# Performance work log

Measured on AMD Instinct MI355X. Metric: run time of the kernel, lower is better.

## Reference

```python
import jax, jax.numpy as jnp
import numpy as np

H, SK, SV, PK, PV = 8, 16, 16, 4, 8
EPS = 1e-8
NUM_LOGITS = 3
SCALE_SCALAR = (NUM_LOGITS * SK) ** -0.5
SCALE_POINT = (NUM_LOGITS * PK * (9.0 / 2.0)) ** -0.5
SCALE_PAIR = NUM_LOGITS ** -0.5


def setup_inputs() -> dict:
    key = jax.random.key(0)
    ks = jax.random.split(key, 16)
    b, n, dim, pdim = 1, 512, 384, 128
    s = 0.02
    return {
        "single_repr": jax.random.normal(ks[0], (b, n, dim), jnp.float32),
        "pairwise_repr": jax.random.normal(ks[1], (b, n, n, pdim), jnp.float32),
        "rotations": jax.random.normal(ks[2], (b, n, 3, 3), jnp.float32),
        "translations": jax.random.normal(ks[3], (b, n, 3), jnp.float32),
        "Wsq": jax.random.normal(ks[4], (dim, H * SK), jnp.float32) * s,
        "Wsk": jax.random.normal(ks[5], (dim, H * SK), jnp.float32) * s,
        "Wsv": jax.random.normal(ks[6], (dim, H * SV), jnp.float32) * s,
        "Wpq": jax.random.normal(ks[7], (dim, H * PK * 3), jnp.float32) * s,
        "Wpk": jax.random.normal(ks[8], (dim, H * PK * 3), jnp.float32) * s,
        "Wpv": jax.random.normal(ks[9], (dim, H * PV * 3), jnp.float32) * s,
        "point_weights": jnp.log(jnp.exp(jnp.ones((H,), jnp.float32)) - 1.0),
        "Wpair": jax.random.normal(ks[10], (pdim, H), jnp.float32) * s,
        "bpair": jnp.zeros((H,), jnp.float32),
        "Wout": jax.random.normal(ks[11], (H * (SV + pdim + PV * 4), dim), jnp.float32) * s,
        "bout": jnp.zeros((dim,), jnp.float32),
    }


def reference(single_repr, pairwise_repr, rotations, translations,
              Wsq, Wsk, Wsv, Wpq, Wpk, Wpv, point_weights, Wpair, bpair, Wout, bout):
    x = single_repr
    b, n, _ = x.shape

    # scalar q/k/v: [b, n, h, d]
    q_s = (x @ Wsq).reshape(b, n, H, SK)
    k_s = (x @ Wsk).reshape(b, n, H, SK)
    v_s = (x @ Wsv).reshape(b, n, H, SV)

    # point q/k/v in local frame: [b, n, h, d, 3], then rotate + translate to global frame
    def to_global(t, d):
        p = t.reshape(b, n, H, d, 3)
        return jnp.einsum('bnhdc,bncr->bnhdr', p, rotations) + translations[:, :, None, None, :]

    q_p = to_global(x @ Wpq, PK)   # [b,n,h,pk,3]
    k_p = to_global(x @ Wpk, PK)
    v_p = to_global(x @ Wpv, PV)   # [b,n,h,pv,3]

    # scalar logits [b,h,i,j]
    logits_scalar = jnp.einsum('bihd,bjhd->bhij', q_s, k_s) * SCALE_SCALAR

    # point-distance logits: sum over (d,c) of (q_i - k_j)^2
    q_ph = jnp.transpose(q_p, (0, 2, 1, 3, 4))  # [b,h,i,pk,3]
    k_ph = jnp.transpose(k_p, (0, 2, 1, 3, 4))
    diff = q_ph[:, :, :, None] - k_ph[:, :, None]          # [b,h,i,j,pk,3]
    dist2 = jnp.sum(diff * diff, axis=(-2, -1))            # [b,h,i,j]
    pw = jax.nn.softplus(point_weights)[None, :, None, None]
    logits_points = -0.5 * pw * SCALE_POINT * dist2

    # pairwise bias logits
    logits_pair = jnp.transpose(pairwise_repr @ Wpair + bpair, (0, 3, 1, 2)) * SCALE_PAIR

    attn = jax.nn.softmax(logits_scalar + logits_points + logits_pair, axis=-1)  # [b,h,i,j]

    # scalar output
    res_scalar = jnp.einsum('bhij,bjhd->bihd', attn, v_s).reshape(b, n, H * SV)

    # pairwise output
    res_pair = jnp.einsum('bhij,bijd->bihd', attn, pairwise_repr).reshape(b, n, -1)

    # point output: attend, then map back to local frame with R^T
    v_ph = jnp.transpose(v_p, (0, 2, 1, 3, 4))             # [b,h,j,pv,3]
    res_p = jnp.einsum('bhij,bhjdc->bhidc', attn, v_ph)    # [b,h,i,pv,3] (global)
    res_p = res_p - translations[:, None, :, None, :]
    res_p = jnp.einsum('bhndc,bnrc->bhndr', res_p, rotations)  # R^T applied
    res_p_norm = jnp.sqrt(jnp.sum(res_p * res_p, axis=-1) + EPS)  # [b,h,n,pv]
    res_p = jnp.transpose(res_p, (0, 2, 1, 3, 4)).reshape(b, n, H * PV * 3)
    res_p_norm = jnp.transpose(res_p_norm, (0, 2, 1, 3)).reshape(b, n, H * PV)

    results = jnp.concatenate([res_scalar, res_p, res_p_norm, res_pair], axis=-1)
    return results @ Wout + bout
```

## Files before the change

### kernel.cpp

```cpp
#include <hip/hip_runtime.h>
#include <math.h>

#define NTOK 512
#define DIM 384
#define PDIM 128
#define H 8

#define QKB_STRIDE 224
#define VB_STRIDE  320
#define RES_STRIDE 1408
#define PART_STRIDE 1360

static constexpr float SCALE_SCALAR = 0.14433756729740643f;
static constexpr float SCALE_POINT  = 0.13608276348795434f;
static constexpr float SCALE_PAIR   = 0.57735026918962580f;

__device__ __forceinline__ float f4get(const float4& v, int k) {
  return (k == 0) ? v.x : (k == 1) ? v.y : (k == 2) ? v.z : v.w;
}

__global__ __launch_bounds__(192) void ipa_proj(
    const float* __restrict__ x, const float* __restrict__ rot, const float* __restrict__ trans,
    const float* __restrict__ Wsq, const float* __restrict__ Wsk, const float* __restrict__ Wsv,
    const float* __restrict__ Wpq, const float* __restrict__ Wpk, const float* __restrict__ Wpv,
    float* __restrict__ qB, float* __restrict__ kB, float* __restrict__ vB)
{
  const int tt = blockIdx.x, cg = blockIdx.y, tid = threadIdx.x;
  __shared__ float s_x[8][DIM];
  __shared__ float s_p[8][192];
  __shared__ float s_R[8][9];
  __shared__ float s_T[8][3];

#pragma unroll
  for (int tok = 0; tok < 8; ++tok)
    for (int k = tid; k < DIM; k += 192) s_x[tok][k] = x[(size_t)(tt * 8 + tok) * DIM + k];
  if (tid < 72) s_R[tid / 9][tid % 9] = rot[(size_t)(tt * 8) * 9 + tid];
  if (tid < 24) s_T[tid / 3][tid % 3] = trans[(size_t)(tt * 8) * 3 + tid];
  __syncthreads();

  const int c = cg * 192 + tid;
  const float* W; int ncols, lc;
  if      (c < 128) { W = Wsq; ncols = 128; lc = c; }
  else if (c < 256) { W = Wsk; ncols = 128; lc = c - 128; }
  else if (c < 384) { W = Wsv; ncols = 128; lc = c - 256; }
  else if (c < 480) { W = Wpq; ncols = 96;  lc = c - 384; }
  else if (c < 576) { W = Wpk; ncols = 96;  lc = c - 480; }
  else              { W = Wpv; ncols = 192; lc = c - 576; }

  float acc[8] = {};
  const float* wp = W + lc;
#pragma unroll 4
  for (int k = 0; k < DIM; ++k) {
    float w = *wp; wp += ncols;
#pragma unroll
    for (int tok = 0; tok < 8; ++tok) acc[tok] += w * s_x[tok][k];
  }

  if (cg < 2) {
#pragma unroll
    for (int tok = 0; tok < 8; ++tok) {
      const int i = tt * 8 + tok;
      if (c < 128)      qB[(size_t)i * QKB_STRIDE + c] = acc[tok];
      else if (c < 256) kB[(size_t)i * QKB_STRIDE + (c - 128)] = acc[tok];
      else              vB[(size_t)i * VB_STRIDE + (c - 256)] = acc[tok];
    }
  } else {
#pragma unroll
    for (int tok = 0; tok < 8; ++tok) s_p[tok][tid] = acc[tok];
    __syncthreads();
    for (int t = tid; t < 512; t += 192) {
      const int tok = t >> 6, tr = t & 63;
      const int i = tt * 8 + tok;
      const float* R = s_R[tok];
      const float* T = s_T[tok];
      const float* src; float* dst;
      if (cg == 2) {
        if (tr < 32) { src = &s_p[tok][tr * 3];            dst = qB + (size_t)i * QKB_STRIDE + 128 + tr * 3; }
        else         { src = &s_p[tok][96 + (tr - 32) * 3]; dst = kB + (size_t)i * QKB_STRIDE + 128 + (tr - 32) * 3; }
      } else {
        src = &s_p[tok][tr * 3]; dst = vB + (size_t)i * VB_STRIDE + 128 + tr * 3;
      }
      float px = src[0], py = src[1], pz = src[2];
#pragma unroll
      for (int r = 0; r < 3; ++r)
        dst[r] = px * R[0 * 3 + r] + py * R[1 * 3 + r] + pz * R[2 * 3 + r] + T[r];
    }
  }
}

__global__ __launch_bounds__(256, 8) void ipa_attn_part(
    const float* __restrict__ pair, const float* __restrict__ pw,
    const float* __restrict__ Wpair, const float* __restrict__ bpair,
    const float* __restrict__ qB, const float* __restrict__ kB,
    const float* __restrict__ vB, float* __restrict__ partial,
    int NC, int JR)
{
  const int i = blockIdx.x, c = blockIdx.y, tid = threadIdx.x;
  extern __shared__ float sm[];
  float* s_attn = sm;
  float* s_red  = s_attn + JR * 12;
  float* s_wp   = s_red + 2048;
  float* s_qs   = s_wp + 1024;
  float* s_qp   = s_qs + 128;
  float* s_coef = s_qp + 96;
  float* s_bp   = s_coef + 8;
  float* s_m    = s_bp + 8;
  float* s_l    = s_m + 8;

  for (int t = tid; t < 1024; t += 256) s_wp[t] = Wpair[t];
  if (tid < 224) {
    float v = qB[(size_t)i * QKB_STRIDE + tid];
    if (tid < 128) s_qs[tid] = v; else s_qp[tid - 128] = v;
  }
  if (tid < 8) {
    s_coef[tid] = -0.5f * log1pf(__expf(pw[tid])) * SCALE_POINT;
    s_bp[tid]   = bpair[tid] * SCALE_PAIR;
  }
  __syncthreads();

  {
    const int half = tid & 1;
    const int hb = half * 4;
    for (int jl = tid >> 1; jl < JR; jl += 128) {
      const int j = c * JR + jl;
      const float4* pr = reinterpret_cast<const float4*>(pair + ((size_t)i * NTOK + j) * PDIM);
      const float4* kb = reinterpret_cast<const float4*>(kB + (size_t)j * QKB_STRIDE);

      float pa[H] = {};
#pragma unroll 4
      for (int d4i = 0; d4i < 16; ++d4i) {
        const int d4 = half * 16 + d4i;
        float4 a = pr[d4];
        const float4* wp = reinterpret_cast<const float4*>(s_wp + d4 * 32);
#pragma unroll
        for (int dd = 0; dd < 4; ++dd) {
          float4 wA = wp[dd * 2], wB = wp[dd * 2 + 1];
          float xv = f4get(a, dd);
          pa[0] += xv * wA.x; pa[1] += xv * wA.y; pa[2] += xv * wA.z; pa[3] += xv * wA.w;
          pa[4] += xv * wB.x; pa[5] += xv * wB.y; pa[6] += xv * wB.z; pa[7] += xv * wB.w;
        }
      }

      float sa[4] = {};
      const float4* q4 = reinterpret_cast<const float4*>(s_qs);
#pragma unroll
      for (int t = 0; t < 16; ++t) {
        const int t4 = half * 16 + t;
        float4 q = q4[t4], k = kb[t4];
        sa[t >> 2] += q.x * k.x + q.y * k.y + q.z * k.z + q.w * k.w;
      }

      float da[4] = {};
      const float4* qp4 = reinterpret_cast<const float4*>(s_qp);
#pragma unroll
      for (int t = 0; t < 12; ++t) {
        const int t4 = half * 12 + t;
        float4 q = qp4[t4], k = kb[32 + t4];
        float d0 = q.x - k.x, d1 = q.y - k.y, d2 = q.z - k.z, d3 = q.w - k.w;
        da[t / 3] += d0 * d0 + d1 * d1 + d2 * d2 + d3 * d3;
      }

      float lg[H];
#pragma unroll
      for (int h = 0; h < H; ++h) lg[h] = pa[h] * SCALE_PAIR;
#pragma unroll
      for (int hh = 0; hh < 4; ++hh)
        lg[hb + hh] += sa[hh] * SCALE_SCALAR + s_coef[hb + hh] * da[hh];
#pragma unroll
      for (int h = 0; h < H; ++h) { float o = __shfl_xor(lg[h], 1); lg[h] += o; }
      if (half == 0) {
#pragma unroll
        for (int h = 0; h < H; ++h) s_attn[jl * 12 + h] = lg[h] + s_bp[h];
      }
    }
  }
  __syncthreads();

  {
    const int h = tid >> 5, l = tid & 31;
    float m = -1e30f;
    for (int k = l; k < JR; k += 32) m = fmaxf(m, s_attn[k * 12 + h]);
#pragma unroll
    for (int off = 16; off; off >>= 1) m = fmaxf(m, __shfl_xor(m, off, 32));
    float s = 0.f;
    for (int k = l; k < JR; k += 32) {
      float e = __expf(s_attn[k * 12 + h] - m);
      s_attn[k * 12 + h] = e;
      s += e;
    }
#pragma unroll
    for (int off = 16; off; off >>= 1) s += __shfl_xor(s, off, 32);
    if (l == 0) { s_m[h] = m; s_l[h] = s; }
  }
  __syncthreads();

  float* part = partial + ((size_t)i * NC + c) * PART_STRIDE;

  {
    const int g = tid >> 5, d4 = tid & 31;
    float4 acc[H];
#pragma unroll
    for (int h = 0; h < H; ++h) acc[h] = make_float4(0.f, 0.f, 0.f, 0.f);
    const float4* pb4 = reinterpret_cast<const float4*>(pair + (size_t)i * NTOK * PDIM);
    const int rpg = JR >> 3;
    for (int jl = g * rpg, e = g * rpg + rpg; jl < e; ++jl) {
      float4 pv = pb4[(size_t)(c * JR + jl) * 32 + d4];
      const float4* ar = reinterpret_cast<const float4*>(s_attn + jl * 12);
      float4 aA = ar[0], aB = ar[1];
#define FMA4(A, S) { (A).x += (S) * pv.x; (A).y += (S) * pv.y; (A).z += (S) * pv.z; (A).w += (S) * pv.w; }
      FMA4(acc[0], aA.x) FMA4(acc[1], aA.y) FMA4(acc[2], aA.z) FMA4(acc[3], aA.w)
      FMA4(acc[4], aB.x) FMA4(acc[5], aB.y) FMA4(acc[6], aB.z) FMA4(acc[7], aB.w)
#undef FMA4
    }
    float* buf = s_red + (g >> 2) * 1024;
    const int rnd = g & 3;
    for (int r = 0; r < 4; ++r) {
      if (rnd == r) {
        if (r == 0) {
#pragma unroll
          for (int h = 0; h < H; ++h)
            *reinterpret_cast<float4*>(buf + h * 128 + d4 * 4) = acc[h];
        } else {
#pragma unroll
          for (int h = 0; h < H; ++h) {
            float4* p = reinterpret_cast<float4*>(buf + h * 128 + d4 * 4);
            float4 v = *p;
            v.x += acc[h].x; v.y += acc[h].y; v.z += acc[h].z; v.w += acc[h].w;
            *p = v;
          }
        }
      }
      __syncthreads();
    }
    float4 v0 = *reinterpret_cast<float4*>(s_red + tid * 4);
    float4 v1 = *reinterpret_cast<float4*>(s_red + 1024 + tid * 4);
    float4 o;
    o.x = v0.x + v1.x; o.y = v0.y + v1.y; o.z = v0.z + v1.z; o.w = v0.w + v1.w;
    *reinterpret_cast<float4*>(part + 336 + tid * 4) = o;
    if (tid < 8) { part[tid] = s_m[tid]; part[8 + tid] = s_l[tid]; }
  }

  {
    const int o = tid;
    const int h0 = (o < 128) ? (o >> 4) : (o - 128) / 24;
    const int o2 = tid + 256;
    const int h1 = (tid < 64) ? (o2 - 128) / 24 : 0;
    float a0 = 0.f, a1 = 0.f;
#pragma unroll 4
    for (int jl = 0; jl < JR; ++jl) {
      const float* vr = vB + (size_t)(c * JR + jl) * VB_STRIDE;
      const float* aw = s_attn + jl * 12;
      a0 += aw[h0] * vr[o];
      if (tid < 64) a1 += aw[h1] * vr[o2];
    }
    if (o < 128) part[16 + o] = a0; else part[144 + (o - 128)] = a0;
    if (tid < 64) part[144 + (o2 - 128)] = a1;
  }
}

__global__ __launch_bounds__(256) void ipa_combine(
    const float* __restrict__ partial, const float* __restrict__ rot,
    const float* __restrict__ trans, float* __restrict__ results, int NC)
{
  const int i = blockIdx.x, tid = threadIdx.x;
  __shared__ float s_f[4][H];
  __shared__ float s_invL[H];
  __shared__ float s_res[RES_STRIDE];
  __shared__ float s_pt[192];
  __shared__ float s_R[9], s_T[3];

  const float* pb = partial + (size_t)i * NC * PART_STRIDE;
  if (tid < H) {
    float M = -1e30f;
    for (int cc = 0; cc < NC; ++cc) M = fmaxf(M, pb[cc * PART_STRIDE + tid]);
    float L = 0.f;
    for (int cc = 0; cc < NC; ++cc) {
      float f = __expf(pb[cc * PART_STRIDE + tid] - M);
      s_f[cc][tid] = f;
      L += f * pb[cc * PART_STRIDE + 8 + tid];
    }
    s_invL[tid] = 1.f / L;
  }
  if (tid >= 32 && tid < 41) s_R[tid - 32] = rot[i * 9 + (tid - 32)];
  if (tid >= 48 && tid < 51) s_T[tid - 48] = trans[i * 3 + (tid - 48)];
  __syncthreads();

  for (int idx = tid; idx < 1344; idx += 256) {
    int h, ofs;
    if (idx < 128)      { h = idx >> 4;          ofs = 16 + idx; }
    else if (idx < 320) { h = (idx - 128) / 24;  ofs = 144 + (idx - 128); }
    else                { h = (idx - 320) >> 7;  ofs = 336 + (idx - 320); }
    float v = 0.f;
    for (int cc = 0; cc < NC; ++cc) v += s_f[cc][h] * pb[cc * PART_STRIDE + ofs];
    v *= s_invL[h];
    if (idx < 128)      s_res[idx] = v;
    else if (idx < 320) s_pt[idx - 128] = v;
    else                s_res[384 + (idx - 320)] = v;
  }
  __syncthreads();

  if (tid < 64) {
    const int h = tid >> 3, p = tid & 7;
    const int base = h * 24 + p * 3;
    float gx = s_pt[base]     - s_T[0];
    float gy = s_pt[base + 1] - s_T[1];
    float gz = s_pt[base + 2] - s_T[2];
    float lx = gx * s_R[0] + gy * s_R[1] + gz * s_R[2];
    float ly = gx * s_R[3] + gy * s_R[4] + gz * s_R[5];
    float lz = gx * s_R[6] + gy * s_R[7] + gz * s_R[8];
    s_res[128 + base]     = lx;
    s_res[128 + base + 1] = ly;
    s_res[128 + base + 2] = lz;
    s_res[320 + h * 8 + p] = sqrtf(lx * lx + ly * ly + lz * lz + 1e-8f);
  }
  __syncthreads();

  float4* dst = reinterpret_cast<float4*>(results + (size_t)i * RES_STRIDE);
  const float4* src = reinterpret_cast<const float4*>(s_res);
  for (int t = tid; t < RES_STRIDE / 4; t += 256) dst[t] = src[t];
}

__global__ __launch_bounds__(256) void ipa_out(
    const float* __restrict__ results, const float* __restrict__ Wout,
    const float* __restrict__ bout, float* __restrict__ out)
{
  const int tt = blockIdx.x, ct = blockIdx.y, tid = threadIdx.x;
  __shared__ float s_a[16][128];
  __shared__ float s_w[128][32];
  const int cc = tid & 31, tr = tid >> 5;
  float acc0 = 0.f, acc1 = 0.f;
  for (int k0 = 0; k0 < RES_STRIDE; k0 += 128) {
    __syncthreads();
    for (int t = tid; t < 512; t += 256) {
      const int tok = t >> 5, k4 = t & 31;
      reinterpret_cast<float4*>(&s_a[tok][0])[k4] =
          *reinterpret_cast<const float4*>(results + (size_t)(tt * 16 + tok) * RES_STRIDE + k0 + k4 * 4);
    }
    for (int t = tid; t < 1024; t += 256) {
      const int kk = t >> 3, c4 = t & 7;
      reinterpret_cast<float4*>(&s_w[kk][0])[c4] =
          *reinterpret_cast<const float4*>(Wout + (size_t)(k0 + kk) * DIM + ct * 32 + c4 * 4);
    }
    __syncthreads();
#pragma unroll 16
    for (int kk = 0; kk < 128; ++kk) {
      float w = s_w[kk][cc];
      acc0 += w * s_a[tr][kk];
      acc1 += w * s_a[tr + 8][kk];
    }
  }
  const float b = bout[ct * 32 + cc];
  out[(size_t)(tt * 16 + tr) * DIM + ct * 32 + cc] = acc0 + b;
  out[(size_t)(tt * 16 + tr + 8) * DIM + ct * 32 + cc] = acc1 + b;
}

extern "C" void kernel_launch(void* const* d_in, const int* in_sizes, int n_in,
                              void* d_out, int out_size, void* d_ws, size_t ws_size,
                              hipStream_t stream) {
  const float* x     = (const float*)d_in[0];
  const float* pair  = (const float*)d_in[1];
  const float* rot   = (const float*)d_in[2];
  const float* trans = (const float*)d_in[3];
  const float* Wsq   = (const float*)d_in[4];
  const float* Wsk   = (const float*)d_in[5];
  const float* Wsv   = (const float*)d_in[6];
  const float* Wpq   = (const float*)d_in[7];
  const float* Wpk   = (const float*)d_in[8];
  const float* Wpv   = (const float*)d_in[9];
  const float* pw    = (const float*)d_in[10];
  const float* Wpair = (const float*)d_in[11];
  const float* bpair = (const float*)d_in[12];
  const float* Wout  = (const float*)d_in[13];
  const float* bout  = (const float*)d_in[14];
  float* out = (float*)d_out;

  float* ws = (float*)d_ws;
  float* qB = ws;
  float* kB = qB + (size_t)NTOK * QKB_STRIDE;
  float* vB = kB + (size_t)NTOK * QKB_STRIDE;
  float* results = vB + (size_t)NTOK * VB_STRIDE;
  float* partial = results + (size_t)NTOK * RES_STRIDE;

  const size_t base_f = (size_t)NTOK * QKB_STRIDE * 2 + (size_t)NTOK * VB_STRIDE
                      + (size_t)NTOK * RES_STRIDE;
  int NC = 4;
  while (NC > 1 && (base_f + (size_t)NTOK * NC * PART_STRIDE) * 4 > ws_size) NC >>= 1;
  const int JR = NTOK / NC;
  const size_t shmem = (size_t)(JR * 12 + 2048 + 1024 + 128 + 96 + 32) * 4;

  ipa_proj<<<dim3(NTOK / 8, 4), 192, 0, stream>>>(x, rot, trans, Wsq, Wsk, Wsv, Wpq, Wpk, Wpv, qB, kB, vB);
  ipa_attn_part<<<dim3(NTOK, NC), 256, shmem, stream>>>(pair, pw, Wpair, bpair, qB, kB, vB, partial, NC, JR);
  ipa_combine<<<NTOK, 256, 0, stream>>>(partial, rot, trans, results, NC);
  ipa_out<<<dim3(NTOK / 16, DIM / 32), 256, 0, stream>>>(results, Wout, bout, out);
}
```

Before: 451.5 us.

## Restructure attention partial kernel into single-pass tiled online softmax over shared pair tiles

The attention-partial kernel now streams the pairwise representation in 64-row tiles through a swizzled shared-memory buffer, prefetching the next tile into registers. Each pair tile is read from global memory once and reused for both the pair-bias logits and the pair-weighted output. Softmax becomes an online max/sum update across tiles, with wavefront shuffles replacing the separate reduction passes. The chunk count rises to 8 and the grid is reordered so chunks of the same row are adjacent. The cost is more register pressure (occupancy hint lowered to 4), extra barriers per tile, and more partials to merge.

```diff
diff --git a/kernel.cpp b/kernel.cpp
--- a/kernel.cpp
+++ b/kernel.cpp
@@ -14,10 +14,6 @@
 static constexpr float SCALE_SCALAR = 0.14433756729740643f;
 static constexpr float SCALE_POINT  = 0.13608276348795434f;
 static constexpr float SCALE_PAIR   = 0.57735026918962580f;
-
-__device__ __forceinline__ float f4get(const float4& v, int k) {
-  return (k == 0) ? v.x : (k == 1) ? v.y : (k == 2) ? v.z : v.w;
-}
 
 __global__ __launch_bounds__(192) void ipa_proj(
     const float* __restrict__ x, const float* __restrict__ rot, const float* __restrict__ trans,
@@ -75,7 +71,7 @@
       const float* T = s_T[tok];
       const float* src; float* dst;
       if (cg == 2) {
-        if (tr < 32) { src = &s_p[tok][tr * 3];            dst = qB + (size_t)i * QKB_STRIDE + 128 + tr * 3; }
+        if (tr < 32) { src = &s_p[tok][tr * 3];             dst = qB + (size_t)i * QKB_STRIDE + 128 + tr * 3; }
         else         { src = &s_p[tok][96 + (tr - 32) * 3]; dst = kB + (size_t)i * QKB_STRIDE + 128 + (tr - 32) * 3; }
       } else {
         src = &s_p[tok][tr * 3]; dst = vB + (size_t)i * VB_STRIDE + 128 + tr * 3;
@@ -88,174 +84,157 @@
   }
 }
 
-__global__ __launch_bounds__(256, 8) void ipa_attn_part(
+__global__ __launch_bounds__(256, 4) void ipa_attn_part(
     const float* __restrict__ pair, const float* __restrict__ pw,
     const float* __restrict__ Wpair, const float* __restrict__ bpair,
     const float* __restrict__ qB, const float* __restrict__ kB,
     const float* __restrict__ vB, float* __restrict__ partial,
-    int NC, int JR)
+    int NC, int JR, int NT)
 {
-  const int i = blockIdx.x, c = blockIdx.y, tid = threadIdx.x;
-  extern __shared__ float sm[];
-  float* s_attn = sm;
-  float* s_red  = s_attn + JR * 12;
-  float* s_wp   = s_red + 2048;
-  float* s_qs   = s_wp + 1024;
-  float* s_qp   = s_qs + 128;
-  float* s_coef = s_qp + 96;
-  float* s_bp   = s_coef + 8;
-  float* s_m    = s_bp + 8;
-  float* s_l    = s_m + 8;
-
-  for (int t = tid; t < 1024; t += 256) s_wp[t] = Wpair[t];
+  const int c = blockIdx.x, i = blockIdx.y, tid = threadIdx.x;
+
+  __shared__ float4 s_pT4[2048];
+  __shared__ float  s_wpT[H][PDIM];
+  __shared__ float  s_e[4][2][64];
+  __shared__ float  s_qs[128];
+  __shared__ float  s_qp[96];
+  __shared__ float  s_coef[H], s_bp[H];
+
+  for (int t = tid; t < PDIM * H; t += 256) {
+    const int h = t >> 7, d = t & 127;
+    s_wpT[h][d] = Wpair[d * 8 + h] * SCALE_PAIR;
+  }
   if (tid < 224) {
     float v = qB[(size_t)i * QKB_STRIDE + tid];
     if (tid < 128) s_qs[tid] = v; else s_qp[tid - 128] = v;
   }
-  if (tid < 8) {
+  if (tid < H) {
     s_coef[tid] = -0.5f * log1pf(__expf(pw[tid])) * SCALE_POINT;
     s_bp[tid]   = bpair[tid] * SCALE_PAIR;
   }
   __syncthreads();
 
+  const int hp = tid >> 6, jl = tid & 63;
+  const int h0 = 2 * hp, h1 = h0 + 1;
+  const int h = tid >> 5, u = tid & 31;
+  const float coef0 = s_coef[h0], coef1 = s_coef[h1];
+  const float bp0 = s_bp[h0], bp1 = s_bp[h1];
+  const int ovb0 = (u < 16) ? (h * 16 + u) : (128 + h * 24 + (u - 16));
+  const int ovb1 = 128 + h * 24 + 16 + u;
+
+  float m0 = -1e30f, m1 = -1e30f, l0 = 0.f, l1 = 0.f;
+  float4 accp = make_float4(0.f, 0.f, 0.f, 0.f);
+  float accv0 = 0.f, accv1 = 0.f;
+
+  float4 r[8];
   {
-    const int half = tid & 1;
-    const int hb = half * 4;
-    for (int jl = tid >> 1; jl < JR; jl += 128) {
-      const int j = c * JR + jl;
-      const float4* pr = reinterpret_cast<const float4*>(pair + ((size_t)i * NTOK + j) * PDIM);
-      const float4* kb = reinterpret_cast<const float4*>(kB + (size_t)j * QKB_STRIDE);
-
-      float pa[H] = {};
-#pragma unroll 4
-      for (int d4i = 0; d4i < 16; ++d4i) {
-        const int d4 = half * 16 + d4i;
-        float4 a = pr[d4];
-        const float4* wp = reinterpret_cast<const float4*>(s_wp + d4 * 32);
-#pragma unroll
-        for (int dd = 0; dd < 4; ++dd) {
-          float4 wA = wp[dd * 2], wB = wp[dd * 2 + 1];
-          float xv = f4get(a, dd);
-          pa[0] += xv * wA.x; pa[1] += xv * wA.y; pa[2] += xv * wA.z; pa[3] += xv * wA.w;
-          pa[4] += xv * wB.x; pa[5] += xv * wB.y; pa[6] += xv * wB.z; pa[7] += xv * wB.w;
-        }
+    const float4* g = reinterpret_cast<const float4*>(pair + ((size_t)i * NTOK + (size_t)c * JR) * PDIM);
+#pragma unroll
+    for (int k = 0; k < 8; ++k) r[k] = g[tid + 256 * k];
+  }
+
+  for (int t = 0; t < NT; ++t) {
+    __syncthreads();
+#pragma unroll
+    for (int k = 0; k < 8; ++k) {
+      const int f = tid + 256 * k;
+      s_pT4[(f & 31) * 64 + ((f >> 5) ^ (f & 7))] = r[k];
+    }
+    __syncthreads();
+    if (t + 1 < NT) {
+      const float4* g = reinterpret_cast<const float4*>(
+          pair + ((size_t)i * NTOK + (size_t)c * JR + (size_t)(t + 1) * 64) * PDIM);
+#pragma unroll
+      for (int k = 0; k < 8; ++k) r[k] = g[tid + 256 * k];
+    }
+
+    float pa0 = 0.f, pa1 = 0.f;
+    {
+      const float4* w0p = reinterpret_cast<const float4*>(&s_wpT[h0][0]);
+      const float4* w1p = reinterpret_cast<const float4*>(&s_wpT[h1][0]);
+#pragma unroll 8
+      for (int d4 = 0; d4 < 32; ++d4) {
+        float4 p = s_pT4[d4 * 64 + (jl ^ (d4 & 7))];
+        float4 w0 = w0p[d4], w1 = w1p[d4];
+        pa0 += p.x * w0.x + p.y * w0.y + p.z * w0.z + p.w * w0.w;
+        pa1 += p.x * w1.x + p.y * w1.y + p.z * w1.z + p.w * w1.w;
       }
-
-      float sa[4] = {};
-      const float4* q4 = reinterpret_cast<const float4*>(s_qs);
-#pragma unroll
-      for (int t = 0; t < 16; ++t) {
-        const int t4 = half * 16 + t;
-        float4 q = q4[t4], k = kb[t4];
-        sa[t >> 2] += q.x * k.x + q.y * k.y + q.z * k.z + q.w * k.w;
+    }
+    const int j = c * JR + t * 64 + jl;
+    const float4* kr4 = reinterpret_cast<const float4*>(kB + (size_t)j * QKB_STRIDE);
+    float sa0 = 0.f, sa1 = 0.f;
+    {
+      const float4* qs4 = reinterpret_cast<const float4*>(s_qs);
+#pragma unroll
+      for (int tq = 0; tq < 4; ++tq) {
+        float4 q = qs4[h0 * 4 + tq], k = kr4[h0 * 4 + tq];
+        sa0 += q.x * k.x + q.y * k.y + q.z * k.z + q.w * k.w;
+        float4 q2 = qs4[h1 * 4 + tq], k2 = kr4[h1 * 4 + tq];
+        sa1 += q2.x * k2.x + q2.y * k2.y + q2.z * k2.z + q2.w * k2.w;
       }
-
-      float da[4] = {};
+    }
+    float da0 = 0.f, da1 = 0.f;
+    {
       const float4* qp4 = reinterpret_cast<const float4*>(s_qp);
 #pragma unroll
-      for (int t = 0; t < 12; ++t) {
-        const int t4 = half * 12 + t;
-        float4 q = qp4[t4], k = kb[32 + t4];
+      for (int tq = 0; tq < 3; ++tq) {
+        float4 q = qp4[h0 * 3 + tq], k = kr4[32 + h0 * 3 + tq];
         float d0 = q.x - k.x, d1 = q.y - k.y, d2 = q.z - k.z, d3 = q.w - k.w;
-        da[t / 3] += d0 * d0 + d1 * d1 + d2 * d2 + d3 * d3;
+        da0 += d0 * d0 + d1 * d1 + d2 * d2 + d3 * d3;
+        float4 q2 = qp4[h1 * 3 + tq], k2 = kr4[32 + h1 * 3 + tq];
+        float e0d = q2.x - k2.x, e1d = q2.y - k2.y, e2d = q2.z - k2.z, e3d = q2.w - k2.w;
+        da1 += e0d * e0d + e1d * e1d + e2d * e2d + e3d * e3d;
       }
-
-      float lg[H];
-#pragma unroll
-      for (int h = 0; h < H; ++h) lg[h] = pa[h] * SCALE_PAIR;
-#pragma unroll
-      for (int hh = 0; hh < 4; ++hh)
-        lg[hb + hh] += sa[hh] * SCALE_SCALAR + s_coef[hb + hh] * da[hh];
-#pragma unroll
-      for (int h = 0; h < H; ++h) { float o = __shfl_xor(lg[h], 1); lg[h] += o; }
-      if (half == 0) {
-#pragma unroll
-        for (int h = 0; h < H; ++h) s_attn[jl * 12 + h] = lg[h] + s_bp[h];
-      }
-    }
-  }
-  __syncthreads();
-
-  {
-    const int h = tid >> 5, l = tid & 31;
-    float m = -1e30f;
-    for (int k = l; k < JR; k += 32) m = fmaxf(m, s_attn[k * 12 + h]);
-#pragma unroll
-    for (int off = 16; off; off >>= 1) m = fmaxf(m, __shfl_xor(m, off, 32));
-    float s = 0.f;
-    for (int k = l; k < JR; k += 32) {
-      float e = __expf(s_attn[k * 12 + h] - m);
-      s_attn[k * 12 + h] = e;
-      s += e;
-    }
-#pragma unroll
-    for (int off = 16; off; off >>= 1) s += __shfl_xor(s, off, 32);
-    if (l == 0) { s_m[h] = m; s_l[h] = s; }
-  }
-  __syncthreads();
+    }
+    float lg0 = sa0 * SCALE_SCALAR + coef0 * da0 + pa0 + bp0;
+    float lg1 = sa1 * SCALE_SCALAR + coef1 * da1 + pa1 + bp1;
+
+    float tm0 = lg0, tm1 = lg1;
+#pragma unroll
+    for (int off = 32; off; off >>= 1) {
+      tm0 = fmaxf(tm0, __shfl_xor(tm0, off, 64));
+      tm1 = fmaxf(tm1, __shfl_xor(tm1, off, 64));
+    }
+    const float m0n = fmaxf(m0, tm0), m1n = fmaxf(m1, tm1);
+    const float sc0 = __expf(m0 - m0n), sc1 = __expf(m1 - m1n);
+    const float e0 = __expf(lg0 - m0n), e1 = __expf(lg1 - m1n);
+    float ts0 = e0, ts1 = e1;
+#pragma unroll
+    for (int off = 32; off; off >>= 1) {
+      ts0 += __shfl_xor(ts0, off, 64);
+      ts1 += __shfl_xor(ts1, off, 64);
+    }
+    m0 = m0n; m1 = m1n;
+    l0 = l0 * sc0 + ts0;
+    l1 = l1 * sc1 + ts1;
+    s_e[hp][0][jl] = e0;
+    s_e[hp][1][jl] = e1;
+
+    const float sc = (tid & 32) ? sc1 : sc0;
+    accp.x *= sc; accp.y *= sc; accp.z *= sc; accp.w *= sc;
+    accv0 *= sc; accv1 *= sc;
+    const float* erow = &s_e[hp][(tid >> 5) & 1][0];
+    const float* vrow = vB + (size_t)(c * JR + t * 64) * VB_STRIDE;
+#pragma unroll 8
+    for (int j2 = 0; j2 < 64; ++j2) {
+      const float e = erow[j2];
+      float4 p = s_pT4[u * 64 + (j2 ^ (u & 7))];
+      accp.x += e * p.x; accp.y += e * p.y; accp.z += e * p.z; accp.w += e * p.w;
+      accv0 += e * vrow[ovb0];
+      if (u < 8) accv1 += e * vrow[ovb1];
+      vrow += VB_STRIDE;
+    }
+  }
 
   float* part = partial + ((size_t)i * NC + c) * PART_STRIDE;
-
-  {
-    const int g = tid >> 5, d4 = tid & 31;
-    float4 acc[H];
-#pragma unroll
-    for (int h = 0; h < H; ++h) acc[h] = make_float4(0.f, 0.f, 0.f, 0.f);
-    const float4* pb4 = reinterpret_cast<const float4*>(pair + (size_t)i * NTOK * PDIM);
-    const int rpg = JR >> 3;
-    for (int jl = g * rpg, e = g * rpg + rpg; jl < e; ++jl) {
-      float4 pv = pb4[(size_t)(c * JR + jl) * 32 + d4];
-      const float4* ar = reinterpret_cast<const float4*>(s_attn + jl * 12);
-      float4 aA = ar[0], aB = ar[1];
-#define FMA4(A, S) { (A).x += (S) * pv.x; (A).y += (S) * pv.y; (A).z += (S) * pv.z; (A).w += (S) * pv.w; }
-      FMA4(acc[0], aA.x) FMA4(acc[1], aA.y) FMA4(acc[2], aA.z) FMA4(acc[3], aA.w)
-      FMA4(acc[4], aB.x) FMA4(acc[5], aB.y) FMA4(acc[6], aB.z) FMA4(acc[7], aB.w)
-#undef FMA4
-    }
-    float* buf = s_red + (g >> 2) * 1024;
-    const int rnd = g & 3;
-    for (int r = 0; r < 4; ++r) {
-      if (rnd == r) {
-        if (r == 0) {
-#pragma unroll
-          for (int h = 0; h < H; ++h)
-            *reinterpret_cast<float4*>(buf + h * 128 + d4 * 4) = acc[h];
-        } else {
-#pragma unroll
-          for (int h = 0; h < H; ++h) {
-            float4* p = reinterpret_cast<float4*>(buf + h * 128 + d4 * 4);
-            float4 v = *p;
-            v.x += acc[h].x; v.y += acc[h].y; v.z += acc[h].z; v.w += acc[h].w;
-            *p = v;
-          }
-        }
-      }
-      __syncthreads();
-    }
-    float4 v0 = *reinterpret_cast<float4*>(s_red + tid * 4);
-    float4 v1 = *reinterpret_cast<float4*>(s_red + 1024 + tid * 4);
-    float4 o;
-    o.x = v0.x + v1.x; o.y = v0.y + v1.y; o.z = v0.z + v1.z; o.w = v0.w + v1.w;
-    *reinterpret_cast<float4*>(part + 336 + tid * 4) = o;
-    if (tid < 8) { part[tid] = s_m[tid]; part[8 + tid] = s_l[tid]; }
-  }
-
-  {
-    const int o = tid;
-    const int h0 = (o < 128) ? (o >> 4) : (o - 128) / 24;
-    const int o2 = tid + 256;
-    const int h1 = (tid < 64) ? (o2 - 128) / 24 : 0;
-    float a0 = 0.f, a1 = 0.f;
-#pragma unroll 4
-    for (int jl = 0; jl < JR; ++jl) {
-      const float* vr = vB + (size_t)(c * JR + jl) * VB_STRIDE;
-      const float* aw = s_attn + jl * 12;
-      a0 += aw[h0] * vr[o];
-      if (tid < 64) a1 += aw[h1] * vr[o2];
-    }
-    if (o < 128) part[16 + o] = a0; else part[144 + (o - 128)] = a0;
-    if (tid < 64) part[144 + (o2 - 128)] = a1;
-  }
+  if ((tid & 63) == 0) {
+    part[h0] = m0; part[h1] = m1;
+    part[8 + h0] = l0; part[8 + h1] = l1;
+  }
+  *reinterpret_cast<float4*>(part + 336 + h * 128 + u * 4) = accp;
+  if (u < 16) part[16 + h * 16 + u] = accv0;
+  else        part[144 + h * 24 + (u - 16)] = accv0;
+  if (u < 8)  part[144 + h * 24 + 16 + u] = accv1;
 }
 
 __global__ __launch_bounds__(256) void ipa_combine(
@@ -263,7 +242,7 @@
     const float* __restrict__ trans, float* __restrict__ results, int NC)
 {
   const int i = blockIdx.x, tid = threadIdx.x;
-  __shared__ float s_f[4][H];
+  __shared__ float s_f[8][H];
   __shared__ float s_invL[H];
   __shared__ float s_res[RES_STRIDE];
   __shared__ float s_pt[192];
@@ -286,13 +265,13 @@
   __syncthreads();
 
   for (int idx = tid; idx < 1344; idx += 256) {
-    int h, ofs;
-    if (idx < 128)      { h = idx >> 4;          ofs = 16 + idx; }
-    else if (idx < 320) { h = (idx - 128) / 24;  ofs = 144 + (idx - 128); }
-    else                { h = (idx - 320) >> 7;  ofs = 336 + (idx - 320); }
+    int hh, ofs;
+    if (idx < 128)      { hh = idx >> 4;          ofs = 16 + idx; }
+    else if (idx < 320) { hh = (idx - 128) / 24;  ofs = 144 + (idx - 128); }
+    else                { hh = (idx - 320) >> 7;  ofs = 336 + (idx - 320); }
     float v = 0.f;
-    for (int cc = 0; cc < NC; ++cc) v += s_f[cc][h] * pb[cc * PART_STRIDE + ofs];
-    v *= s_invL[h];
+    for (int cc = 0; cc < NC; ++cc) v += s_f[cc][hh] * pb[cc * PART_STRIDE + ofs];
+    v *= s_invL[hh];
     if (idx < 128)      s_res[idx] = v;
     else if (idx < 320) s_pt[idx - 128] = v;
     else                s_res[384 + (idx - 320)] = v;
@@ -300,8 +279,8 @@
   __syncthreads();
 
   if (tid < 64) {
-    const int h = tid >> 3, p = tid & 7;
-    const int base = h * 24 + p * 3;
+    const int hh = tid >> 3, p = tid & 7;
+    const int base = hh * 24 + p * 3;
     float gx = s_pt[base]     - s_T[0];
     float gy = s_pt[base + 1] - s_T[1];
     float gz = s_pt[base + 2] - s_T[2];
@@ -311,7 +290,7 @@
     s_res[128 + base]     = lx;
     s_res[128 + base + 1] = ly;
     s_res[128 + base + 2] = lz;
-    s_res[320 + h * 8 + p] = sqrtf(lx * lx + ly * ly + lz * lz + 1e-8f);
+    s_res[320 + hh * 8 + p] = sqrtf(lx * lx + ly * ly + lz * lz + 1e-8f);
   }
   __syncthreads();
 
@@ -383,13 +362,13 @@
 
   const size_t base_f = (size_t)NTOK * QKB_STRIDE * 2 + (size_t)NTOK * VB_STRIDE
                       + (size_t)NTOK * RES_STRIDE;
-  int NC = 4;
+  int NC = 8;
   while (NC > 1 && (base_f + (size_t)NTOK * NC * PART_STRIDE) * 4 > ws_size) NC >>= 1;
   const int JR = NTOK / NC;
-  const size_t shmem = (size_t)(JR * 12 + 2048 + 1024 + 128 + 96 + 32) * 4;
+  const int NT = JR / 64;
 
   ipa_proj<<<dim3(NTOK / 8, 4), 192, 0, stream>>>(x, rot, trans, Wsq, Wsk, Wsv, Wpq, Wpk, Wpv, qB, kB, vB);
-  ipa_attn_part<<<dim3(NTOK, NC), 256, shmem, stream>>>(pair, pw, Wpair, bpair, qB, kB, vB, partial, NC, JR);
+  ipa_attn_part<<<dim3(NC, NTOK), 256, 0, stream>>>(pair, pw, Wpair, bpair, qB, kB, vB, partial, NC, JR, NT);
   ipa_combine<<<NTOK, 256, 0, stream>>>(partial, rot, trans, results, NC);
   ipa_out<<<dim3(NTOK / 16, DIM / 32), 256, 0, stream>>>(results, Wout, bout, out);
 }
```

Measured after the change: 476.7 us. 5.6% more time.
